# Optimization experiments

Hardware: AMD Instinct MI355X
Metric: run time of the kernel (lower is better)

## Reference

```python
import jax, jax.numpy as jnp
import numpy as np

B, SEQ, DIM = 32, 512, 1024
DEPTH, HEADS, DHEAD = 6, 8, 64
INNER = HEADS * DHEAD  # 512
NLAT, MAXSEQ = 64, 512
EPS = 1e-5


def setup_inputs() -> dict:
    key = jax.random.key(0)
    ks = jax.random.split(key, 8)
    return {
        "x": jax.random.normal(ks[0], (B, SEQ, DIM), dtype=jnp.float32),
        "attention_mask": jax.random.randint(ks[1], (B, SEQ), 0, 2, dtype=jnp.int32),
        "latents": jax.random.normal(ks[2], (NLAT, DIM), dtype=jnp.float32),
        "media_pos_emb": jax.random.normal(ks[3], (MAXSEQ, DIM), dtype=jnp.float32),
        "ln_media_g": jnp.ones((DEPTH, DIM), jnp.float32),
        "ln_media_b": jnp.zeros((DEPTH, DIM), jnp.float32),
        "ln_lat_g": jnp.ones((DEPTH, DIM), jnp.float32),
        "ln_lat_b": jnp.zeros((DEPTH, DIM), jnp.float32),
        "Wq": jax.random.normal(ks[4], (DEPTH, DIM, INNER), dtype=jnp.float32) * 0.02,
        "Wkv": jax.random.normal(ks[5], (DEPTH, DIM, 2 * INNER), dtype=jnp.float32) * 0.02,
        "Wout": jax.random.normal(ks[6], (DEPTH, INNER, DIM), dtype=jnp.float32) * 0.02,
        "final_g": jnp.ones((DIM,), jnp.float32),
        "final_b": jnp.zeros((DIM,), jnp.float32),
    }


def _layer_norm(x, g, b):
    mu = jnp.mean(x, axis=-1, keepdims=True)
    var = jnp.mean(jnp.square(x - mu), axis=-1, keepdims=True)
    return (x - mu) * jax.lax.rsqrt(var + EPS) * g + b


def _heads(t):
    # b n (h d) -> b h n d
    b, n, _ = t.shape
    return t.reshape(b, n, HEADS, DHEAD).transpose(0, 2, 1, 3)


def reference(x, attention_mask, latents, media_pos_emb, ln_media_g, ln_media_b,
              ln_lat_g, ln_lat_b, Wq, Wkv, Wout, final_g, final_b):
    b, seq, _ = x.shape
    x = x + media_pos_emb[None, :seq, :]
    lat = jnp.broadcast_to(latents[None], (b, NLAT, DIM))
    scale = DHEAD ** -0.5
    # key mask over [latents ++ media]: latent keys never masked; 1 == masked
    key_mask = jnp.concatenate(
        [jnp.zeros((b, NLAT), attention_mask.dtype), attention_mask], axis=1)
    masked = (key_mask == 1)[:, None, None, :]  # b 1 1 j
    for l in range(DEPTH):
        xm = _layer_norm(x, ln_media_g[l], ln_media_b[l])
        ln = _layer_norm(lat, ln_lat_g[l], ln_lat_b[l])
        q = _heads(ln @ Wq[l])                      # b h i d
        kv = jnp.concatenate([ln, xm], axis=1) @ Wkv[l]
        k, v = jnp.split(kv, 2, axis=-1)
        k, v = _heads(k), _heads(v)                 # b h j d
        sim = jnp.einsum('bhid,bhjd->bhij', q * scale, k)
        sim = jnp.where(masked, -jnp.inf, sim)
        attn = jax.nn.softmax(sim, axis=-1)
        out = jnp.einsum('bhij,bhjd->bhid', attn, v)
        out = out.transpose(0, 2, 1, 3).reshape(b, NLAT, INNER)
        lat = lat + out @ Wout[l]
    return _layer_norm(lat, final_g, final_b)
```

## Files before the change

kernel.cpp:

```cpp
#include <hip/hip_runtime.h>
#include <cstdint>


#define DEVINL __device__ __forceinline__

typedef __attribute__((ext_vector_type(8))) short short8_t;
typedef __attribute__((ext_vector_type(4))) float f32x4;

DEVINL ushort f2bf(float f) {
  union { float f; uint32_t u; } c; c.f = f;
  uint32_t u = c.u;
  u += ((u >> 16) & 1u) + 0x7fffu;
  return (ushort)(u >> 16);
}
DEVINL float bf2f(ushort u) {
  union { uint32_t u; float f; } c; c.u = ((uint32_t)u) << 16;
  return c.f;
}
DEVINL f32x4 mfma16(short8_t a, short8_t b, f32x4 c) {
  return __builtin_amdgcn_mfma_f32_16x16x32_bf16(a, b, c, 0, 0, 0);
}
DEVINL void gld16(ushort* lds, const ushort* g) {
  __builtin_amdgcn_global_load_lds(
      (const __attribute__((address_space(1))) void*)g,
      (__attribute__((address_space(3))) void*)lds, 16, 0, 0);
}

__global__ __launch_bounds__(256, 2) void k_gemm128m(const ushort* __restrict__ A,
    const ushort* __restrict__ Bt, const float* __restrict__ bias,
    ushort* __restrict__ Kb, ushort* __restrict__ Vt) {
  extern __shared__ char lds[];
  constexpr int K = 1024, NT = 16;
  int tid = threadIdx.x, lane = tid & 63, w = tid >> 6;
  int wr = w >> 1, wc = w & 1;
  int fr = lane & 15;
  int fkb = (lane >> 4) << 4;
  int xorv = (fr & 7) << 4;
  int bid = blockIdx.x;
  int xcd = bid & 7, ii = bid >> 3;
  int m0 = (xcd * 16 + (ii >> 3)) * 128;
  int n0 = (ii & 7) * 128;
  int sce = ((lane & 7) ^ (lane >> 3)) << 3;
  const ushort* Ag = A + (size_t)(m0 + w * 32 + (lane >> 3)) * K + sce;
  const ushort* Bg = Bt + (size_t)(n0 + w * 32 + (lane >> 3)) * K + sce;
  f32x4 acc[4][4] = {};

  auto stA = [&](int t) {
    char* d = lds + (t % 3) * 16384 + w * 4096;
    const ushort* s = Ag + t * 64;
#pragma unroll
    for (int g = 0; g < 4; ++g)
      gld16((ushort*)(d + g * 1024), s + (size_t)(g * 8) * K);
  };
  auto stB = [&](int t) {
    char* d = lds + 49152 + (t & 1) * 16384 + w * 4096;
    const ushort* s = Bg + t * 64;
#pragma unroll
    for (int g = 0; g < 4; ++g)
      gld16((ushort*)(d + g * 1024), s + (size_t)(g * 8) * K);
  };
  stA(0); stB(0); stA(1);

  for (int t = 0; t < NT; ++t) {
    const char* ab = lds + (t % 3) * 16384;
    const char* bb = lds + 49152 + (t & 1) * 16384;
    if (t + 1 < NT) asm volatile("s_waitcnt vmcnt(4)" ::: "memory");
    else            asm volatile("s_waitcnt vmcnt(0)" ::: "memory");
    __builtin_amdgcn_s_barrier();
    short8_t a[4][2], b[4][2];
#pragma unroll
    for (int mt = 0; mt < 4; ++mt)
#pragma unroll
      for (int kh = 0; kh < 2; ++kh)
        a[mt][kh] = *(const short8_t*)(ab +
            ((wr * 64 + mt * 16 + fr) << 7) + ((kh * 64 + fkb) ^ xorv));
#pragma unroll
    for (int nt = 0; nt < 4; ++nt)
#pragma unroll
      for (int kh = 0; kh < 2; ++kh)
        b[nt][kh] = *(const short8_t*)(bb +
            ((wc * 64 + nt * 16 + fr) << 7) + ((kh * 64 + fkb) ^ xorv));
    if (t + 1 < NT) stB(t + 1);
    if (t + 2 < NT) stA(t + 2);
    __builtin_amdgcn_s_setprio(1);
#pragma unroll
    for (int kh = 0; kh < 2; ++kh)
#pragma unroll
      for (int mt = 0; mt < 4; ++mt)
#pragma unroll
        for (int nt = 0; nt < 4; ++nt)
          acc[mt][nt] = mfma16(a[mt][kh], b[nt][kh], acc[mt][nt]);
    __builtin_amdgcn_s_setprio(0);
    __builtin_amdgcn_s_barrier();
  }

  __syncthreads();
  ushort* Cl = (ushort*)lds;
  constexpr int CLS = 136;
  bool isV = (n0 >= 512);
#pragma unroll
  for (int mt = 0; mt < 4; ++mt)
#pragma unroll
    for (int nt = 0; nt < 4; ++nt)
#pragma unroll
      for (int r = 0; r < 4; ++r) {
        int rl = wr * 64 + mt * 16 + ((lane >> 4) << 2) + r;
        int cl = wc * 64 + nt * 16 + fr;
        ushort v = f2bf(acc[mt][nt][r] + bias[n0 + cl]);
        if (!isV) Cl[rl * CLS + cl] = v;
        else      Cl[cl * CLS + rl] = v;
      }
  __syncthreads();
  int b_ = m0 >> 9;
  int jb = 64 + (m0 & 511);
#pragma unroll
  for (int q2 = 0; q2 < 8; ++q2) {
    int task = tid + q2 * 256;
    int rr2 = task >> 4, c8 = task & 15;
    short8_t vv = *(const short8_t*)&Cl[rr2 * CLS + c8 * 8];
    if (!isV)
      *(short8_t*)&Kb[((size_t)(b_ * 576 + jb + rr2) << 9) + n0 + c8 * 8] = vv;
    else
      *(short8_t*)&Vt[(size_t)(b_ * 512 + (n0 - 512) + rr2) * 576 + jb + c8 * 8] = vv;
  }
}

__global__ __launch_bounds__(512) void k_attn(const ushort* __restrict__ Q,
    const ushort* __restrict__ Kb, const ushort* __restrict__ Vt,
    const int* __restrict__ amask, ushort* __restrict__ AO) {
  extern __shared__ char alds[];
  ushort* sim = (ushort*)alds;
  char* stg = alds + 74752;
  int bh = blockIdx.x;
  int h = bh & 7, b = bh >> 3;
  int tid = threadIdx.x, lane = tid & 63, w = tid >> 6;
  int rg = w >> 1, ch = w & 1;
  int fr = lane & 15;
  int fkb = (lane >> 4) << 4;
  int csrc8 = ((lane & 7) ^ (lane >> 3)) << 3;
  short8_t aq0, aq1;
  {
    int qi = rg * 16 + fr;
    const ushort* qp = Q + ((size_t)(b * 64 + qi) << 9) + h * 64 + ((lane >> 4) << 3);
    aq0 = *(const short8_t*)qp;
    aq1 = *(const short8_t*)(qp + 32);
  }
  unsigned mbits = 0;
#pragma unroll
  for (int c = 1; c < 9; ++c)
    if (amask[b * 512 + (c - 1) * 64 + lane]) mbits |= (1u << c);

  auto stageK = [&](int it, int buf) {
#pragma unroll
    for (int g = 0; g < 3; ++g) {
      int sr = w * 24 + g * 8 + (lane >> 3);
      ushort* d = (ushort*)(stg + buf * 24576 + (w * 24 + g * 8) * 128);
      gld16(d, Kb + ((size_t)(b * 576 + it * 192 + sr) << 9) + h * 64 + csrc8);
    }
  };
  auto stageV = [&](int it, int buf) {
#pragma unroll
    for (int g = 0; g < 3; ++g) {
      int sr = w * 8 + (lane >> 3);
      ushort* d = (ushort*)(stg + buf * 24576 + g * 8192 + w * 8 * 128);
      gld16(d, Vt + (size_t)(b * 512 + h * 64 + sr) * 576 + it * 192 + g * 64 + csrc8);
    }
  };

  stageK(0, 0);
  for (int it = 0; it < 3; ++it) {
    int buf = it & 1;
    __builtin_amdgcn_s_barrier();
    if (it + 1 < 3) {
      stageK(it + 1, buf ^ 1);
      asm volatile("s_waitcnt vmcnt(3)" ::: "memory");
    } else {
      asm volatile("s_waitcnt vmcnt(0)" ::: "memory");
    }
    __builtin_amdgcn_s_barrier();
    const char* kb_ = stg + buf * 24576;
#pragma unroll
    for (int ct = 0; ct < 6; ++ct) {
      int row_l = ch * 96 + ct * 16 + fr;
      const char* base = kb_ + row_l * 128;
      int sw = (row_l & 7) << 4;
      short8_t k0 = *(const short8_t*)(base + (fkb ^ sw));
      short8_t k1 = *(const short8_t*)(base + ((64 + fkb) ^ sw));
      f32x4 s4 = {};
      s4 = mfma16(aq0, k0, s4);
      s4 = mfma16(aq1, k1, s4);
#pragma unroll
      for (int r = 0; r < 4; ++r)
        sim[(rg * 16 + ((lane >> 4) << 2) + r) * 584 +
            it * 192 + ch * 96 + ct * 16 + fr] = f2bf(s4[r]);
    }
  }
  __syncthreads();
  stageV(0, 0);
  for (int rr = 0; rr < 8; ++rr) {
    int row = w * 8 + rr;
    float vals[9];
    float m = -3.0e38f;
#pragma unroll
    for (int c = 0; c < 9; ++c) {
      float v = bf2f(sim[row * 584 + c * 64 + lane]);
      vals[c] = v;
      if (!((mbits >> c) & 1)) m = fmaxf(m, v);
    }
#pragma unroll
    for (int off = 32; off; off >>= 1) m = fmaxf(m, __shfl_xor(m, off));
    float ssum = 0.f;
    float p[9];
#pragma unroll
    for (int c = 0; c < 9; ++c) {
      p[c] = ((mbits >> c) & 1) ? 0.f : __expf(vals[c] - m);
      ssum += p[c];
    }
#pragma unroll
    for (int off = 32; off; off >>= 1) ssum += __shfl_xor(ssum, off);
    float inv = 1.0f / ssum;
#pragma unroll
    for (int c = 0; c < 9; ++c)
      sim[row * 584 + c * 64 + lane] = f2bf(p[c] * inv);
  }
  __syncthreads();
  f32x4 oacc[2] = {};
  for (int it = 0; it < 3; ++it) {
    int buf = it & 1;
    __builtin_amdgcn_s_barrier();
    if (it + 1 < 3) {
      stageV(it + 1, buf ^ 1);
      asm volatile("s_waitcnt vmcnt(3)" ::: "memory");
    } else {
      asm volatile("s_waitcnt vmcnt(0)" ::: "memory");
    }
    __builtin_amdgcn_s_barrier();
#pragma unroll
    for (int g = 0; g < 3; ++g) {
      const char* vb_ = stg + buf * 24576 + g * 8192;
      const ushort* srow_ = &sim[(rg * 16 + fr) * 584 + it * 192 + g * 64];
      short8_t pa0 = *(const short8_t*)(srow_ + ((lane >> 4) << 3));
      short8_t pa1 = *(const short8_t*)(srow_ + 32 + ((lane >> 4) << 3));
#pragma unroll
      for (int dt = 0; dt < 2; ++dt) {
        int row_l = ch * 32 + dt * 16 + fr;
        const char* base = vb_ + row_l * 128;
        int sw = (row_l & 7) << 4;
        short8_t v0 = *(const short8_t*)(base + (fkb ^ sw));
        short8_t v1 = *(const short8_t*)(base + ((64 + fkb) ^ sw));
        oacc[dt] = mfma16(pa0, v0, oacc[dt]);
        oacc[dt] = mfma16(pa1, v1, oacc[dt]);
      }
    }
  }
#pragma unroll
  for (int dt = 0; dt < 2; ++dt)
#pragma unroll
    for (int r = 0; r < 4; ++r) {
      int i = rg * 16 + ((lane >> 4) << 2) + r;
      int d = ch * 32 + dt * 16 + fr;
      AO[((size_t)(b * 64 + i) << 9) + h * 64 + d] = f2bf(oacc[dt][r]);
    }
}

__global__ __launch_bounds__(256) void k_fold_kv(const float* __restrict__ Wkv,
    const float* __restrict__ lnmg, const float* __restrict__ lnlg,
    const float* __restrict__ lnmb, const float* __restrict__ lnlb,
    ushort* __restrict__ wkvmT, ushort* __restrict__ wlatT,
    float* __restrict__ pb) {
  __shared__ float tile[32][33];
  __shared__ float pm[8][32], pl[8][32];
  int l = blockIdx.z, rt = blockIdx.y;
  int c0 = blockIdx.x * 32, r0 = rt * 32;
  const float* Wl = Wkv + (size_t)l * 1048576;
  int tx = threadIdx.x & 31, ty = threadIdx.x >> 5;
#pragma unroll
  for (int i = 0; i < 4; ++i)
    tile[ty + i * 8][tx] = Wl[(size_t)(r0 + ty + i * 8) * 1024 + c0 + tx];
  __syncthreads();
  float am = 0.f, al = 0.f;
#pragma unroll
  for (int i = 0; i < 4; ++i) {
    int r = ty * 4 + i;
    float wv = tile[r][tx];
    am += lnmb[l * 1024 + r0 + r] * wv;
    al += lnlb[l * 1024 + r0 + r] * wv;
  }
  pm[ty][tx] = am; pl[ty][tx] = al;
#pragma unroll
  for (int i = 0; i < 4; ++i) {
    int c = ty + i * 8;
    float wv = tile[tx][c];
    int r = r0 + tx;
    wkvmT[(size_t)l * 1048576 + (size_t)(c0 + c) * 1024 + r] =
        f2bf(wv * lnmg[l * 1024 + r]);
    wlatT[(size_t)l * 1572864 + (size_t)(512 + c0 + c) * 1024 + r] =
        f2bf(wv * lnlg[l * 1024 + r]);
  }
  __syncthreads();
  if (ty == 0) {
    float sm = 0.f, sl = 0.f;
#pragma unroll
    for (int k = 0; k < 8; ++k) { sm += pm[k][tx]; sl += pl[k][tx]; }
    pb[(size_t)(l * 32 + rt) * 2560 + c0 + tx] = sm;
    pb[(size_t)(l * 32 + rt) * 2560 + 1536 + c0 + tx] = sl;
  }
}

__global__ __launch_bounds__(256) void k_fold_q(const float* __restrict__ Wq,
    const float* __restrict__ lnlg, const float* __restrict__ lnlb,
    ushort* __restrict__ wlatT, float* __restrict__ pb) {
  __shared__ float tile[32][33];
  __shared__ float pq[8][32];
  int l = blockIdx.z, rt = blockIdx.y;
  int c0 = blockIdx.x * 32, r0 = rt * 32;
  const float* Wl = Wq + (size_t)l * 524288;
  int tx = threadIdx.x & 31, ty = threadIdx.x >> 5;
#pragma unroll
  for (int i = 0; i < 4; ++i)
    tile[ty + i * 8][tx] = Wl[(size_t)(r0 + ty + i * 8) * 512 + c0 + tx];
  __syncthreads();
  float aq = 0.f;
#pragma unroll
  for (int i = 0; i < 4; ++i) {
    int r = ty * 4 + i;
    aq += lnlb[l * 1024 + r0 + r] * tile[r][tx];
  }
  pq[ty][tx] = aq;
#pragma unroll
  for (int i = 0; i < 4; ++i) {
    int c = ty + i * 8;
    float wv = tile[tx][c];
    int r = r0 + tx;
    wlatT[(size_t)l * 1572864 + (size_t)(c0 + c) * 1024 + r] =
        f2bf(wv * lnlg[l * 1024 + r] * 0.125f);
  }
  __syncthreads();
  if (ty == 0) {
    float s = 0.f;
#pragma unroll
    for (int k = 0; k < 8; ++k) s += pq[k][tx];
    pb[(size_t)(l * 32 + rt) * 2560 + 1024 + c0 + tx] = s;
  }
}

__global__ __launch_bounds__(256) void k_bias_red(const float* __restrict__ pb,
    float* __restrict__ bkvm, float* __restrict__ blat) {
  int l = blockIdx.y;
  int c = blockIdx.x * 256 + threadIdx.x;
  float s = 0.f;
  for (int rt = 0; rt < 32; ++rt)
    s += pb[(size_t)(l * 32 + rt) * 2560 + c];
  if (c < 1024)       bkvm[l * 1024 + c] = s;
  else if (c < 1536)  blat[l * 1536 + (c - 1024)] = s * 0.125f;
  else                blat[l * 1536 + 512 + (c - 1536)] = s;
}

__global__ __launch_bounds__(256) void k_fold_out(const float* __restrict__ Wout,
    ushort* __restrict__ woutT) {
  __shared__ float tile[32][33];
  int l = blockIdx.z;
  const float* Wl = Wout + (size_t)l * 524288;
  int r0 = blockIdx.y * 32, c0 = blockIdx.x * 32;
  int tx = threadIdx.x & 31, ty = threadIdx.x >> 5;
#pragma unroll
  for (int i = 0; i < 4; ++i)
    tile[ty + i * 8][tx] = Wl[(size_t)(r0 + ty + i * 8) * 1024 + c0 + tx];
  __syncthreads();
#pragma unroll
  for (int i = 0; i < 4; ++i) {
    int jl = ty + i * 8;
    woutT[(size_t)l * 524288 + (size_t)(c0 + jl) * 512 + r0 + tx] = f2bf(tile[tx][jl]);
  }
}

__global__ __launch_bounds__(256) void k_rownorm(const float* __restrict__ in,
    const float* __restrict__ pos, ushort* __restrict__ out) {
  int row = blockIdx.x, t = threadIdx.x;
  float4 v = *(const float4*)(in + (size_t)row * 1024 + t * 4);
  if (pos) {
    float4 p = *(const float4*)(pos + (size_t)(row & 511) * 1024 + t * 4);
    v.x += p.x; v.y += p.y; v.z += p.z; v.w += p.w;
  }
  float s = v.x + v.y + v.z + v.w;
  float q = v.x * v.x + v.y * v.y + v.z * v.z + v.w * v.w;
#pragma unroll
  for (int off = 32; off; off >>= 1) { s += __shfl_xor(s, off); q += __shfl_xor(q, off); }
  __shared__ float rs[4], rq[4];
  if ((t & 63) == 0) { rs[t >> 6] = s; rq[t >> 6] = q; }
  __syncthreads();
  s = rs[0] + rs[1] + rs[2] + rs[3];
  q = rq[0] + rq[1] + rq[2] + rq[3];
  float mean = s * (1.0f / 1024.0f);
  float var = q * (1.0f / 1024.0f) - mean * mean;
  float rstd = rsqrtf(var + 1e-5f);
  ushort4 o;
  o.x = f2bf((v.x - mean) * rstd);
  o.y = f2bf((v.y - mean) * rstd);
  o.z = f2bf((v.z - mean) * rstd);
  o.w = f2bf((v.w - mean) * rstd);
  *(ushort4*)(out + (size_t)row * 1024 + t * 4) = o;
}

__global__ __launch_bounds__(256) void k_finalln(const float* __restrict__ in,
    const float* __restrict__ g, const float* __restrict__ b, float* __restrict__ out) {
  int row = blockIdx.x, t = threadIdx.x;
  float4 v = *(const float4*)(in + (size_t)row * 1024 + t * 4);
  float s = v.x + v.y + v.z + v.w;
  float q = v.x * v.x + v.y * v.y + v.z * v.z + v.w * v.w;
#pragma unroll
  for (int off = 32; off; off >>= 1) { s += __shfl_xor(s, off); q += __shfl_xor(q, off); }
  __shared__ float rs[4], rq[4];
  if ((t & 63) == 0) { rs[t >> 6] = s; rq[t >> 6] = q; }
  __syncthreads();
  s = rs[0] + rs[1] + rs[2] + rs[3];
  q = rq[0] + rq[1] + rq[2] + rq[3];
  float mean = s * (1.0f / 1024.0f);
  float var = q * (1.0f / 1024.0f) - mean * mean;
  float rstd = rsqrtf(var + 1e-5f);
  float4 g4 = *(const float4*)(g + t * 4);
  float4 b4 = *(const float4*)(b + t * 4);
  float4 o;
  o.x = (v.x - mean) * rstd * g4.x + b4.x;
  o.y = (v.y - mean) * rstd * g4.y + b4.y;
  o.z = (v.z - mean) * rstd * g4.z + b4.z;
  o.w = (v.w - mean) * rstd * g4.w + b4.w;
  *(float4*)(out + (size_t)row * 1024 + t * 4) = o;
}

__global__ __launch_bounds__(256) void k_latinit(const float* __restrict__ latents,
                                                 float* __restrict__ lat) {
  int row = blockIdx.x, t = threadIdx.x;
  *(float4*)(lat + (size_t)row * 1024 + t * 4) =
      *(const float4*)(latents + (size_t)(row & 63) * 1024 + t * 4);
}

template <int MODE>
__global__ __launch_bounds__(256) void k_gemm64(const ushort* __restrict__ A,
    const ushort* __restrict__ Bt, const float* __restrict__ bias,
    ushort* __restrict__ o0, ushort* __restrict__ o1, ushort* __restrict__ o2,
    float* __restrict__ of, int N, int K) {
  __shared__ ushort Al[2][64][32];
  __shared__ ushort Bl[2][64][32];
  __shared__ ushort Cl[64][72];
  int tid = threadIdx.x, lane = tid & 63, w = tid >> 6;
  int wr = w >> 1, wc = w & 1;
  int m0 = blockIdx.y * 64, n0 = blockIdx.x * 64;
  f32x4 acc[2][2] = {};
  const ushort* Ag = A + (size_t)(m0 + w * 16 + (lane >> 2)) * K + (lane & 3) * 8;
  const ushort* Bg = Bt + (size_t)(n0 + w * 16 + (lane >> 2)) * K + (lane & 3) * 8;
  int fr = lane & 15, fk = (lane >> 4) << 3;
  int nt = K >> 5;
  gld16(&Al[0][w * 16][0], Ag);
  gld16(&Bl[0][w * 16][0], Bg);
  for (int t = 0; t < nt; ++t) {
    int cur = t & 1;
    if (t + 1 < nt) {
      int k0 = (t + 1) << 5;
      gld16(&Al[cur ^ 1][w * 16][0], Ag + k0);
      gld16(&Bl[cur ^ 1][w * 16][0], Bg + k0);
      asm volatile("s_waitcnt vmcnt(2)" ::: "memory");
    } else {
      asm volatile("s_waitcnt vmcnt(0)" ::: "memory");
    }
    __builtin_amdgcn_s_barrier();
    short8_t a[2], b[2];
#pragma unroll
    for (int mt = 0; mt < 2; ++mt)
      a[mt] = *(const short8_t*)&Al[cur][wr * 32 + mt * 16 + fr][fk];
#pragma unroll
    for (int nt2 = 0; nt2 < 2; ++nt2)
      b[nt2] = *(const short8_t*)&Bl[cur][wc * 32 + nt2 * 16 + fr][fk];
#pragma unroll
    for (int mt = 0; mt < 2; ++mt)
#pragma unroll
      for (int nt2 = 0; nt2 < 2; ++nt2)
        acc[mt][nt2] = mfma16(a[mt], b[nt2], acc[mt][nt2]);
    __builtin_amdgcn_s_barrier();
  }
  if constexpr (MODE == 3) {
    if (n0 >= 1024) {
#pragma unroll
      for (int mt = 0; mt < 2; ++mt)
#pragma unroll
        for (int nt2 = 0; nt2 < 2; ++nt2)
#pragma unroll
          for (int r = 0; r < 4; ++r) {
            int rl = wr * 32 + mt * 16 + ((lane >> 4) << 2) + r;
            int col = wc * 32 + nt2 * 16 + (lane & 15);
            Cl[rl][col] = f2bf(acc[mt][nt2][r] + bias[n0 + col]);
          }
      __syncthreads();
      int b_ = m0 >> 6;
#pragma unroll
      for (int q = 0; q < 2; ++q) {
        int task = tid + q * 256;
        int jg = task & 7, d = task >> 3;
        short8_t vv;
#pragma unroll
        for (int e = 0; e < 8; ++e) vv[e] = (short)Cl[jg * 8 + e][d];
        *(short8_t*)&o2[((size_t)(b_ * 512 + (n0 - 1024) + d)) * 576 + jg * 8] = vv;
      }
      return;
    }
  }
#pragma unroll
  for (int mt = 0; mt < 2; ++mt)
#pragma unroll
    for (int nt2 = 0; nt2 < 2; ++nt2)
#pragma unroll
      for (int r = 0; r < 4; ++r) {
        int row = m0 + wr * 32 + mt * 16 + ((lane >> 4) << 2) + r;
        int col = n0 + wc * 32 + nt2 * 16 + (lane & 15);
        float v = acc[mt][nt2][r] + (bias ? bias[col] : 0.0f);
        if constexpr (MODE == 3) {
          int b_ = row >> 6, ii = row & 63;
          if (col < 512) o0[(size_t)row * 512 + col] = f2bf(v);
          else           o1[(((size_t)(b_ * 576 + ii)) << 9) + (col - 512)] = f2bf(v);
        } else {
          of[(size_t)row * N + col] += v;
        }
      }
}

extern "C" void kernel_launch(void* const* d_in, const int* in_sizes, int n_in,
                              void* d_out, int out_size, void* d_ws, size_t ws_size,
                              hipStream_t stream) {
  const float* x       = (const float*)d_in[0];
  const int*   amask   = (const int*)d_in[1];
  const float* latents = (const float*)d_in[2];
  const float* pos     = (const float*)d_in[3];
  const float* lnmg    = (const float*)d_in[4];
  const float* lnmb    = (const float*)d_in[5];
  const float* lnlg    = (const float*)d_in[6];
  const float* lnlb    = (const float*)d_in[7];
  const float* Wq      = (const float*)d_in[8];
  const float* Wkv     = (const float*)d_in[9];
  const float* Wout    = (const float*)d_in[10];
  const float* fg      = (const float*)d_in[11];
  const float* fb      = (const float*)d_in[12];
  float* out = (float*)d_out;
  char* ws = (char*)d_ws;

  ushort* xhat  = (ushort*)(ws + 0);
  ushort* wkvmT = (ushort*)(ws + 33554432);
  ushort* wlatT = (ushort*)(ws + 46137344);
  ushort* woutT = (ushort*)(ws + 65011712);
  float*  bkvm  = (float*)(ws + 71303168);
  float*  blat  = (float*)(ws + 71327744);
  float*  lat   = (float*)(ws + 71364608);
  ushort* lhat  = (ushort*)(ws + 79753216);
  ushort* qbuf  = (ushort*)(ws + 83947520);
  ushort* Kbuf  = (ushort*)(ws + 86044672);
  ushort* Vt    = (ushort*)(ws + 104919040);
  ushort* aobuf = (ushort*)(ws + 123793408);
  float*  pb    = (float*)(ws + 125890560);

  (void)hipFuncSetAttribute((const void*)k_gemm128m,
                            hipFuncAttributeMaxDynamicSharedMemorySize, 81920);
  (void)hipFuncSetAttribute((const void*)k_attn,
                            hipFuncAttributeMaxDynamicSharedMemorySize, 131072);

  dim3 B256(256);
  k_fold_kv<<<dim3(32, 32, 6), B256, 0, stream>>>(Wkv, lnmg, lnlg, lnmb, lnlb,
                                                  wkvmT, wlatT, pb);
  k_fold_q<<<dim3(16, 32, 6), B256, 0, stream>>>(Wq, lnlg, lnlb, wlatT, pb);
  k_fold_out<<<dim3(32, 16, 6), B256, 0, stream>>>(Wout, woutT);
  k_bias_red<<<dim3(10, 6), B256, 0, stream>>>(pb, bkvm, blat);
  k_rownorm<<<16384, B256, 0, stream>>>(x, pos, xhat);
  k_latinit<<<2048, B256, 0, stream>>>(latents, lat);

  for (int l = 0; l < 6; ++l) {
    k_rownorm<<<2048, B256, 0, stream>>>(lat, nullptr, lhat);
    k_gemm64<3><<<dim3(24, 32), B256, 0, stream>>>(
        lhat, wlatT + (size_t)l * 1572864, blat + l * 1536,
        qbuf, Kbuf, Vt, nullptr, 1536, 1024);
    k_gemm128m<<<dim3(1024), B256, 81920, stream>>>(
        xhat, wkvmT + (size_t)l * 1048576, bkvm + l * 1024, Kbuf, Vt);
    k_attn<<<dim3(256), dim3(512), 123904, stream>>>(qbuf, Kbuf, Vt, amask, aobuf);
    k_gemm64<2><<<dim3(16, 32), B256, 0, stream>>>(
        aobuf, woutT + (size_t)l * 524288, nullptr,
        nullptr, nullptr, nullptr, lat, 1024, 512);
  }
  k_finalln<<<2048, B256, 0, stream>>>(lat, fg, fb, out);
}
```

Measured before the change: 635.9 us.

## Enlarge media KV GEMM tile to 256x128 with K=32 steps

Reworks the media K/V projection GEMM from 128x128 tiles with 64-wide K steps to 256x128 tiles with 32-wide K steps. Each wave now computes 128x64 outputs (8x4 MFMA tiles), which raises arithmetic intensity per loaded B tile and halves the grid to 512 blocks. LDS use drops to 64KB, and the epilogue writes back in two 128-row halves through a staging buffer. The costs are higher accumulator register pressure, twice as many barrier iterations, and a possible loss of occupancy or tail balance.

```diff
diff --git a/kernel.cpp b/kernel.cpp
--- a/kernel.cpp
+++ b/kernel.cpp
@@ -26,70 +26,66 @@
       (__attribute__((address_space(3))) void*)lds, 16, 0, 0);
 }
 
-__global__ __launch_bounds__(256, 2) void k_gemm128m(const ushort* __restrict__ A,
+__global__ __launch_bounds__(256, 2) void k_gemmM(const ushort* __restrict__ A,
     const ushort* __restrict__ Bt, const float* __restrict__ bias,
     ushort* __restrict__ Kb, ushort* __restrict__ Vt) {
   extern __shared__ char lds[];
-  constexpr int K = 1024, NT = 16;
+  constexpr int K = 1024, NT = 32;
   int tid = threadIdx.x, lane = tid & 63, w = tid >> 6;
-  int wr = w >> 1, wc = w & 1;
+  int wm = w >> 1, wn = w & 1;
   int fr = lane & 15;
-  int fkb = (lane >> 4) << 4;
-  int xorv = (fr & 7) << 4;
+  int c16 = lane >> 4;
+  int xorc = (fr >> 1) & 3;
   int bid = blockIdx.x;
   int xcd = bid & 7, ii = bid >> 3;
-  int m0 = (xcd * 16 + (ii >> 3)) * 128;
+  int m0 = (xcd * 8 + (ii >> 3)) * 256;
   int n0 = (ii & 7) * 128;
-  int sce = ((lane & 7) ^ (lane >> 3)) << 3;
-  const ushort* Ag = A + (size_t)(m0 + w * 32 + (lane >> 3)) * K + sce;
-  const ushort* Bg = Bt + (size_t)(n0 + w * 32 + (lane >> 3)) * K + sce;
-  f32x4 acc[4][4] = {};
+  int ksrc = ((lane & 3) ^ ((lane >> 3) & 3)) << 3;
+  const ushort* Ag = A + (size_t)(m0 + (lane >> 2)) * K + ksrc;
+  const ushort* Bg = Bt + (size_t)(n0 + (lane >> 2)) * K + ksrc;
+  f32x4 acc[8][4] = {};
 
   auto stA = [&](int t) {
     char* d = lds + (t % 3) * 16384 + w * 4096;
-    const ushort* s = Ag + t * 64;
+    const ushort* s = Ag + (size_t)(w * 64) * K + t * 32;
 #pragma unroll
     for (int g = 0; g < 4; ++g)
-      gld16((ushort*)(d + g * 1024), s + (size_t)(g * 8) * K);
+      gld16((ushort*)(d + g * 1024), s + (size_t)(g * 16) * K);
   };
   auto stB = [&](int t) {
-    char* d = lds + 49152 + (t & 1) * 16384 + w * 4096;
-    const ushort* s = Bg + t * 64;
-#pragma unroll
-    for (int g = 0; g < 4; ++g)
-      gld16((ushort*)(d + g * 1024), s + (size_t)(g * 8) * K);
+    char* d = lds + 49152 + (t & 1) * 8192 + w * 2048;
+    const ushort* s = Bg + (size_t)(w * 32) * K + t * 32;
+#pragma unroll
+    for (int g = 0; g < 2; ++g)
+      gld16((ushort*)(d + g * 1024), s + (size_t)(g * 16) * K);
   };
   stA(0); stB(0); stA(1);
 
   for (int t = 0; t < NT; ++t) {
     const char* ab = lds + (t % 3) * 16384;
-    const char* bb = lds + 49152 + (t & 1) * 16384;
+    const char* bb = lds + 49152 + (t & 1) * 8192;
     if (t + 1 < NT) asm volatile("s_waitcnt vmcnt(4)" ::: "memory");
     else            asm volatile("s_waitcnt vmcnt(0)" ::: "memory");
     __builtin_amdgcn_s_barrier();
-    short8_t a[4][2], b[4][2];
-#pragma unroll
-    for (int mt = 0; mt < 4; ++mt)
-#pragma unroll
-      for (int kh = 0; kh < 2; ++kh)
-        a[mt][kh] = *(const short8_t*)(ab +
-            ((wr * 64 + mt * 16 + fr) << 7) + ((kh * 64 + fkb) ^ xorv));
-#pragma unroll
-    for (int nt = 0; nt < 4; ++nt)
-#pragma unroll
-      for (int kh = 0; kh < 2; ++kh)
-        b[nt][kh] = *(const short8_t*)(bb +
-            ((wc * 64 + nt * 16 + fr) << 7) + ((kh * 64 + fkb) ^ xorv));
+    short8_t a[8], b[4];
+#pragma unroll
+    for (int mt = 0; mt < 8; ++mt) {
+      int rl = wm * 128 + mt * 16 + fr;
+      a[mt] = *(const short8_t*)(ab + rl * 64 + ((c16 ^ xorc) << 4));
+    }
+#pragma unroll
+    for (int nt = 0; nt < 4; ++nt) {
+      int rl = wn * 64 + nt * 16 + fr;
+      b[nt] = *(const short8_t*)(bb + rl * 64 + ((c16 ^ xorc) << 4));
+    }
     if (t + 1 < NT) stB(t + 1);
     if (t + 2 < NT) stA(t + 2);
     __builtin_amdgcn_s_setprio(1);
 #pragma unroll
-    for (int kh = 0; kh < 2; ++kh)
-#pragma unroll
-      for (int mt = 0; mt < 4; ++mt)
-#pragma unroll
-        for (int nt = 0; nt < 4; ++nt)
-          acc[mt][nt] = mfma16(a[mt][kh], b[nt][kh], acc[mt][nt]);
+    for (int mt = 0; mt < 8; ++mt)
+#pragma unroll
+      for (int nt = 0; nt < 4; ++nt)
+        acc[mt][nt] = mfma16(a[mt], b[nt], acc[mt][nt]);
     __builtin_amdgcn_s_setprio(0);
     __builtin_amdgcn_s_barrier();
   }
@@ -98,30 +94,44 @@
   ushort* Cl = (ushort*)lds;
   constexpr int CLS = 136;
   bool isV = (n0 >= 512);
-#pragma unroll
-  for (int mt = 0; mt < 4; ++mt)
-#pragma unroll
-    for (int nt = 0; nt < 4; ++nt)
-#pragma unroll
-      for (int r = 0; r < 4; ++r) {
-        int rl = wr * 64 + mt * 16 + ((lane >> 4) << 2) + r;
-        int cl = wc * 64 + nt * 16 + fr;
-        ushort v = f2bf(acc[mt][nt][r] + bias[n0 + cl]);
-        if (!isV) Cl[rl * CLS + cl] = v;
-        else      Cl[cl * CLS + rl] = v;
-      }
-  __syncthreads();
   int b_ = m0 >> 9;
   int jb = 64 + (m0 & 511);
-#pragma unroll
-  for (int q2 = 0; q2 < 8; ++q2) {
-    int task = tid + q2 * 256;
-    int rr2 = task >> 4, c8 = task & 15;
-    short8_t vv = *(const short8_t*)&Cl[rr2 * CLS + c8 * 8];
-    if (!isV)
-      *(short8_t*)&Kb[((size_t)(b_ * 576 + jb + rr2) << 9) + n0 + c8 * 8] = vv;
-    else
-      *(short8_t*)&Vt[(size_t)(b_ * 512 + (n0 - 512) + rr2) * 576 + jb + c8 * 8] = vv;
+  for (int p = 0; p < 2; ++p) {
+    if (p) __syncthreads();
+    if (wm == p) {
+#pragma unroll
+      for (int mt = 0; mt < 8; ++mt)
+#pragma unroll
+        for (int nt = 0; nt < 4; ++nt)
+#pragma unroll
+          for (int r = 0; r < 4; ++r) {
+            int rl = mt * 16 + ((lane >> 4) << 2) + r;
+            int cl = wn * 64 + nt * 16 + fr;
+            ushort v = f2bf(acc[mt][nt][r] + bias[n0 + cl]);
+            if (!isV) Cl[rl * CLS + cl] = v;
+            else      Cl[cl * CLS + rl] = v;
+          }
+    }
+    __syncthreads();
+    if (!isV) {
+#pragma unroll
+      for (int q = 0; q < 8; ++q) {
+        int task = tid + q * 256;
+        int rr = task >> 4, ck = task & 15;
+        short8_t vv = *(const short8_t*)&Cl[rr * CLS + ck * 8];
+        *(short8_t*)&Kb[((size_t)(b_ * 576 + jb + p * 128 + rr) << 9) +
+                        n0 + ck * 8] = vv;
+      }
+    } else {
+#pragma unroll
+      for (int q = 0; q < 8; ++q) {
+        int task = tid + q * 256;
+        int d = task >> 4, jc = task & 15;
+        short8_t vv = *(const short8_t*)&Cl[d * CLS + jc * 8];
+        *(short8_t*)&Vt[(size_t)(b_ * 512 + (n0 - 512) + d) * 576 +
+                        jb + p * 128 + jc * 8] = vv;
+      }
+    }
   }
 }
 
@@ -556,8 +566,8 @@
   ushort* aobuf = (ushort*)(ws + 123793408);
   float*  pb    = (float*)(ws + 125890560);
 
-  (void)hipFuncSetAttribute((const void*)k_gemm128m,
-                            hipFuncAttributeMaxDynamicSharedMemorySize, 81920);
+  (void)hipFuncSetAttribute((const void*)k_gemmM,
+                            hipFuncAttributeMaxDynamicSharedMemorySize, 65536);
   (void)hipFuncSetAttribute((const void*)k_attn,
                             hipFuncAttributeMaxDynamicSharedMemorySize, 131072);
 
@@ -575,7 +585,7 @@
     k_gemm64<3><<<dim3(24, 32), B256, 0, stream>>>(
         lhat, wlatT + (size_t)l * 1572864, blat + l * 1536,
         qbuf, Kbuf, Vt, nullptr, 1536, 1024);
-    k_gemm128m<<<dim3(1024), B256, 81920, stream>>>(
+    k_gemmM<<<dim3(512), B256, 65536, stream>>>(
         xhat, wkvmT + (size_t)l * 1048576, bkvm + l * 1024, Kbuf, Vt);
     k_attn<<<dim3(256), dim3(512), 123904, stream>>>(qbuf, Kbuf, Vt, amask, aobuf);
     k_gemm64<2><<<dim3(16, 32), B256, 0, stream>>>(
```

After: 662.0 us. +4.1%, slower.
